# Kernel optimization log

Hardware: AMD Instinct MI355X
Metric: run time of the kernel (lower is better)

## Reference

```python
import jax, jax.numpy as jnp
import numpy as np

HIDDEN = 1024
NUM_HEADS = 16
D_HEAD = HIDDEN // NUM_HEADS  # 64
SEQ = 2048
BATCH = 2


def setup_inputs() -> dict:
    key = jax.random.key(0)
    kx, kw, kb = jax.random.split(key, 3)
    x = jax.random.normal(kx, (SEQ, BATCH, HIDDEN), dtype=jnp.float32)
    W = jax.random.normal(kw, (3 * HIDDEN, HIDDEN), dtype=jnp.float32) * 0.02
    b = jax.random.normal(kb, (3 * HIDDEN,), dtype=jnp.float32) * 0.02
    return {"x": x, "W": W, "b": b}


def reference(x, W, b):
    # x: (S, B, H) seq-first, as in the torch module
    S, B, _ = x.shape
    qkv = jnp.einsum('sbh,oh->sbo', x, W) + b  # (S, B, 3*H)
    # torch views 3*hidden as (num_heads, 3, d_head): per-head-interleaved QKV
    qkv = qkv.reshape(S, B, NUM_HEADS, 3, D_HEAD)
    qkv = jnp.transpose(qkv, (2, 1, 0, 3, 4))  # (nh, B, S, 3, d)
    q, k, v = qkv[..., 0, :], qkv[..., 1, :], qkv[..., 2, :]  # each (nh, B, S, d)
    scale = 1.0 / np.sqrt(D_HEAD).astype(np.float32)
    scores = jnp.einsum('hbqd,hbkd->hbqk', q, k) * scale  # (nh, B, S, S)
    attn = jax.nn.softmax(scores, axis=-1)
    out = jnp.einsum('hbqk,hbkd->hbqd', attn, v)  # (nh, B, S, d)
    out = jnp.transpose(out, (2, 1, 0, 3)).reshape(S, B, HIDDEN)
    return out
```

## Files before the change

kernel.cpp:

```cpp
#include <hip/hip_runtime.h>
#include <hip/hip_bf16.h>


typedef __hip_bfloat16 bf16;
typedef __bf16 bfr;
typedef __attribute__((ext_vector_type(8))) __bf16 bf16x8;
typedef __attribute__((ext_vector_type(4))) __bf16 bf16x4;
typedef __attribute__((ext_vector_type(2))) __bf16 bf16x2;
typedef __attribute__((ext_vector_type(4))) float f32x4;
typedef __attribute__((ext_vector_type(16))) float f32x16;
typedef __attribute__((ext_vector_type(4))) unsigned u32x4;

#define S_SEQ  2048
#define HID    1024
#define OUT3   3072
#define NROWS  4096

#if __has_builtin(__builtin_amdgcn_exp2f)
#define EXP2F(x) __builtin_amdgcn_exp2f(x)
#else
#define EXP2F(x) exp2f(x)
#endif

#define QSCALE 0.18033688011112042f

__global__ __launch_bounds__(256) void cast_both_kernel(
    const float* __restrict__ X, bfr* __restrict__ Xb,
    const float* __restrict__ W, bfr* __restrict__ Wb)
{
    int bid = blockIdx.x;
    const float* src;
    bfr* dst;
    int lid;
    if (bid < NROWS * HID / 2048) { src = X; dst = Xb; lid = bid; }
    else { src = W; dst = Wb; lid = bid - NROWS * HID / 2048; }
    int gid = lid * 256 + threadIdx.x;
    const float4* s4 = (const float4*)src;
    float4 a = s4[(size_t)gid * 2];
    float4 b = s4[(size_t)gid * 2 + 1];
    bf16x8 v;
    v[0] = (bfr)a.x; v[1] = (bfr)a.y; v[2] = (bfr)a.z; v[3] = (bfr)a.w;
    v[4] = (bfr)b.x; v[5] = (bfr)b.y; v[6] = (bfr)b.z; v[7] = (bfr)b.w;
    *(bf16x8*)(dst + (size_t)gid * 8) = v;
}

__device__ __forceinline__ void gload_lds16(const void* g, void* l) {
    __builtin_amdgcn_global_load_lds(
        (const __attribute__((address_space(1))) unsigned int*)g,
        (__attribute__((address_space(3))) unsigned int*)l, 16, 0, 0);
}

__global__ __launch_bounds__(256, 3) void qkv_gemm_mfma(
    const bfr* __restrict__ Xb, const bfr* __restrict__ Wb,
    const float* __restrict__ bias,
    bfr* __restrict__ qb, bfr* __restrict__ kb, bfr* __restrict__ vtb)
{
    __shared__ __attribute__((aligned(16))) unsigned char lds_all[32768];
    bfr* As = (bfr*)lds_all;
    bfr* Bs = (bfr*)(lds_all + 16384);
    bfr* Tr = (bfr*)lds_all;

    const int o0 = blockIdx.x * 128;
    const int r0 = blockIdx.y * 128;
    const int tid = threadIdx.x;
    const int lane = tid & 63;
    const int w = tid >> 6;
    const int l15 = lane & 15;
    const int quad = lane >> 4;
    const int m0 = (w & 1) * 64;
    const int n0 = (w >> 1) * 64;

    f32x4 acc[4][4];
#pragma unroll
    for (int mi = 0; mi < 4; mi++)
#pragma unroll
        for (int ni = 0; ni < 4; ni++) acc[mi][ni] = {0.f, 0.f, 0.f, 0.f};

    for (int k0 = 0; k0 < HID; k0 += 64) {
#pragma unroll
        for (int i = 0; i < 4; i++) {
            int c = i * 256 + tid;
            int row = c >> 3, c8 = c & 7;
            gload_lds16(Xb + (size_t)(r0 + row) * HID + k0 + c8 * 8, As + c * 8);
            gload_lds16(Wb + (size_t)(o0 + row) * HID + k0 + c8 * 8, Bs + c * 8);
        }
        __syncthreads();

#pragma unroll
        for (int ks = 0; ks < 2; ks++) {
            bf16x8 af[4], bfg[4];
#pragma unroll
            for (int mi = 0; mi < 4; mi++)
                af[mi] = *(const bf16x8*)(As + (m0 + mi * 16 + l15) * 64 + ks * 32 + quad * 8);
#pragma unroll
            for (int ni = 0; ni < 4; ni++)
                bfg[ni] = *(const bf16x8*)(Bs + (n0 + ni * 16 + l15) * 64 + ks * 32 + quad * 8);
#pragma unroll
            for (int mi = 0; mi < 4; mi++)
#pragma unroll
                for (int ni = 0; ni < 4; ni++)
                    acc[mi][ni] = __builtin_amdgcn_mfma_f32_16x16x32_bf16(
                        af[mi], bfg[ni], acc[mi][ni], 0, 0, 0);
        }
        __syncthreads();
    }

    const int omod = o0 % 192;
#pragma unroll
    for (int ni = 0; ni < 4; ni++) {
        int cb = o0 + n0 + ni * 16;
        int h = cb / 192;
        int rem = cb % 192;
        int t = rem >> 6;
        int d = (rem & 63) + l15;
        float bv = bias[cb + l15];
        if (t == 2) {
#pragma unroll
            for (int mi = 0; mi < 4; mi++)
#pragma unroll
                for (int r = 0; r < 4; r++) {
                    int grl = m0 + mi * 16 + quad * 4 + r;
                    Tr[(size_t)d * 144 + (grl & 1) * 72 + (grl >> 1)]
                        = (bfr)(acc[mi][ni][r] + bv);
                }
        } else {
#pragma unroll
            for (int mi = 0; mi < 4; mi++)
#pragma unroll
                for (int r = 0; r < 4; r++) {
                    int gr = r0 + m0 + mi * 16 + quad * 4 + r;
                    int s = gr >> 1, b = gr & 1;
                    int hb = h * 2 + b;
                    float val = acc[mi][ni][r] + bv;
                    if (t == 0)
                        qb[((size_t)hb * S_SEQ + s) * 64 + d] = (bfr)(val * QSCALE);
                    else
                        kb[((size_t)hb * S_SEQ + s) * 64 + d] = (bfr)val;
                }
        }
    }
    if (omod != 0) {
        __syncthreads();
        int ht = (omod == 64) ? (o0 + 64) / 192 : o0 / 192;
        int d = tid >> 2;
        int b = (tid >> 1) & 1;
        int chunk = tid & 1;
        int s0 = r0 >> 1;
        int hb = ht * 2 + b;
        const bfr* src = Tr + (size_t)d * 144 + b * 72 + chunk * 32;
        bfr* dstp = vtb + ((size_t)hb * 64 + d) * S_SEQ + s0 + chunk * 32;
#pragma unroll
        for (int j = 0; j < 4; j++)
            *(bf16x8*)(dstp + j * 8) = *(const bf16x8*)(src + j * 8);
    }
}

__device__ __forceinline__ void plswap(unsigned &a, unsigned &b) {
    asm volatile("v_permlane32_swap_b32 %0, %1" : "+v"(a), "+v"(b));
}

__global__ __launch_bounds__(256, 2) void attn32_kernel(
    const bfr* __restrict__ qb, const bfr* __restrict__ kb,
    const bfr* __restrict__ vtb, float* __restrict__ out)
{
    __shared__ __attribute__((aligned(16))) bfr KV[2][2][64 * 64];

    constexpr int NT = 32;
    const int qt = blockIdx.x;
    const int hb = blockIdx.y;
    const int h = hb >> 1, b = hb & 1;
    const int tid = threadIdx.x;
    const int lane = tid & 63;
    const int w = tid >> 6;
    const int l31 = lane & 31;
    const int hi = lane >> 5;
    const size_t hboff = (size_t)hb * S_SEQ * 64;

    const int srow = tid >> 3;
    const int slot = tid & 7;

    const int qrow = qt * 128 + w * 32 + l31;
    bf16x8 qf[4];
#pragma unroll
    for (int kk = 0; kk < 4; kk++)
        qf[kk] = *(const bf16x8*)(qb + hboff + (size_t)qrow * 64 + kk * 16 + hi * 8);

    f32x16 Oacc[2];
#pragma unroll
    for (int dt = 0; dt < 2; dt++)
#pragma unroll
        for (int i = 0; i < 16; i++) Oacc[dt][i] = 0.f;
    float lsum = 0.f;

#define STAGE(t_) do {                                                         \
    int kt__ = (t_); int bf__ = kt__ & 1;                                      \
    _Pragma("unroll")                                                          \
    for (int i = 0; i < 2; i++) {                                              \
        int r = i * 32 + srow;                                                 \
        int gc = slot ^ (r & 7);                                               \
        gload_lds16(kb + hboff + (size_t)(kt__ * 64 + r) * 64 + gc * 8,        \
                    (bfr*)&KV[bf__][0][0] + i * 2048 + tid * 8);               \
    }                                                                          \
    _Pragma("unroll")                                                          \
    for (int i = 0; i < 2; i++) {                                              \
        int r = i * 32 + srow;                                                 \
        int gc = slot ^ (r & 7);                                               \
        gload_lds16(vtb + hboff + (size_t)r * S_SEQ + kt__ * 64 + gc * 8,      \
                    (bfr*)&KV[bf__][1][0] + i * 2048 + tid * 8);               \
    }                                                                          \
} while (0)

    STAGE(0);

    for (int t = 0; t < NT; t++) {
        asm volatile("s_waitcnt vmcnt(0)" ::: "memory");
        __builtin_amdgcn_s_barrier();
        if (t + 1 < NT) STAGE(t + 1);

        const bfr* Kb = &KV[t & 1][0][0];
        const bfr* Vb = &KV[t & 1][1][0];

        unsigned wds[2][8];
        float rs = 0.f;
#pragma unroll
        for (int ts = 0; ts < 2; ts++) {
            const int krow = ts * 32 + l31;
            f32x16 sc;
#pragma unroll
            for (int i = 0; i < 16; i++) sc[i] = 0.f;
#pragma unroll
            for (int kk = 0; kk < 4; kk++) {
                int ks = (kk * 2 + hi) ^ (krow & 7);
                bf16x8 kf = *(const bf16x8*)(Kb + krow * 64 + ks * 8);
                sc = __builtin_amdgcn_mfma_f32_32x32x16_bf16(kf, qf[kk], sc, 0, 0, 0);
            }
#pragma unroll
            for (int a = 0; a < 8; a++) {
                float p0 = EXP2F(sc[2 * a]);
                float p1 = EXP2F(sc[2 * a + 1]);
                rs += p0 + p1;
                bf16x2 pk; pk[0] = (bfr)p0; pk[1] = (bfr)p1;
                wds[ts][a] = __builtin_bit_cast(unsigned, pk);
            }
        }
        lsum += rs;

        bf16x8 pfrag[4];
#pragma unroll
        for (int c = 0; c < 4; c++) {
            int ts = c >> 1, cc = c & 1;
            unsigned w0 = wds[ts][cc * 4 + 0];
            unsigned w1 = wds[ts][cc * 4 + 1];
            unsigned w2 = wds[ts][cc * 4 + 2];
            unsigned w3 = wds[ts][cc * 4 + 3];
            plswap(w0, w2);
            plswap(w1, w3);
            u32x4 pw; pw[0] = w0; pw[1] = w1; pw[2] = w2; pw[3] = w3;
            pfrag[c] = __builtin_bit_cast(bf16x8, pw);
        }

#pragma unroll
        for (int kk = 0; kk < 4; kk++)
#pragma unroll
            for (int dt = 0; dt < 2; dt++) {
                int vrow = dt * 32 + l31;
                int vs = (kk * 2 + hi) ^ (vrow & 7);
                bf16x8 vf = *(const bf16x8*)(Vb + vrow * 64 + vs * 8);
                Oacc[dt] = __builtin_amdgcn_mfma_f32_32x32x16_bf16(vf, pfrag[kk], Oacc[dt], 0, 0, 0);
            }
    }
#undef STAGE

    lsum += __shfl_xor(lsum, 32);
    float inv = 1.0f / lsum;
    float* orow = out + ((size_t)qrow * 2 + b) * HID + h * 64;
#pragma unroll
    for (int dt = 0; dt < 2; dt++)
#pragma unroll
        for (int g = 0; g < 4; g++) {
            float4 o4;
            o4.x = Oacc[dt][4 * g + 0] * inv;
            o4.y = Oacc[dt][4 * g + 1] * inv;
            o4.z = Oacc[dt][4 * g + 2] * inv;
            o4.w = Oacc[dt][4 * g + 3] * inv;
            *(float4*)(orow + dt * 32 + 8 * g + 4 * hi) = o4;
        }
}

extern "C" void kernel_launch(void* const* d_in, const int* in_sizes, int n_in,
                              void* d_out, int out_size, void* d_ws, size_t ws_size,
                              hipStream_t stream) {
    const float* X    = (const float*)d_in[0];
    const float* W    = (const float*)d_in[1];
    const float* bias = (const float*)d_in[2];
    float* out = (float*)d_out;

    bfr* qb  = (bfr*)d_ws;
    bfr* kb  = qb + (size_t)32 * S_SEQ * 64;
    bfr* vtb = kb + (size_t)32 * S_SEQ * 64;

    bfr* Xb = (bfr*)d_out;
    bfr* Wb = Xb + (size_t)NROWS * HID;

    cast_both_kernel<<<(NROWS * HID + OUT3 * HID) / 2048, 256, 0, stream>>>(X, Xb, W, Wb);

    dim3 g1(OUT3 / 128, NROWS / 128);
    qkv_gemm_mfma<<<g1, 256, 0, stream>>>(Xb, Wb, bias, qb, kb, vtb);

    dim3 g2(S_SEQ / 128, 32);
    attn32_kernel<<<g2, 256, 0, stream>>>(qb, kb, vtb, out);
}
```

Measured before the change: 157.7 us.

## Process two 32-row query tiles per wave in attention, halving block threads

Measured after the change: 175.3 us. 1.11x slower.

```diff
diff --git a/kernel.cpp b/kernel.cpp
--- a/kernel.cpp
+++ b/kernel.cpp
@@ -159,7 +159,7 @@
     asm volatile("v_permlane32_swap_b32 %0, %1" : "+v"(a), "+v"(b));
 }
 
-__global__ __launch_bounds__(256, 2) void attn32_kernel(
+__global__ __launch_bounds__(128, 2) void attn32_kernel(
     const bfr* __restrict__ qb, const bfr* __restrict__ kb,
     const bfr* __restrict__ vtb, float* __restrict__ out)
 {
@@ -179,34 +179,39 @@
     const int srow = tid >> 3;
     const int slot = tid & 7;
 
-    const int qrow = qt * 128 + w * 32 + l31;
-    bf16x8 qf[4];
-#pragma unroll
-    for (int kk = 0; kk < 4; kk++)
-        qf[kk] = *(const bf16x8*)(qb + hboff + (size_t)qrow * 64 + kk * 16 + hi * 8);
-
-    f32x16 Oacc[2];
+    const int qbase = qt * 128 + w * 64;
+    bf16x8 qf[2][4];
+#pragma unroll
+    for (int qh = 0; qh < 2; qh++)
+#pragma unroll
+        for (int kk = 0; kk < 4; kk++)
+            qf[qh][kk] = *(const bf16x8*)(qb + hboff
+                + (size_t)(qbase + qh * 32 + l31) * 64 + kk * 16 + hi * 8);
+
+    f32x16 Oacc[2][2];
 #pragma unroll
     for (int dt = 0; dt < 2; dt++)
 #pragma unroll
-        for (int i = 0; i < 16; i++) Oacc[dt][i] = 0.f;
-    float lsum = 0.f;
+        for (int qh = 0; qh < 2; qh++)
+#pragma unroll
+            for (int i = 0; i < 16; i++) Oacc[dt][qh][i] = 0.f;
+    float lsum0 = 0.f, lsum1 = 0.f;
 
 #define STAGE(t_) do {                                                         \
     int kt__ = (t_); int bf__ = kt__ & 1;                                      \
     _Pragma("unroll")                                                          \
-    for (int i = 0; i < 2; i++) {                                              \
-        int r = i * 32 + srow;                                                 \
+    for (int i = 0; i < 4; i++) {                                              \
+        int r = i * 16 + srow;                                                 \
         int gc = slot ^ (r & 7);                                               \
         gload_lds16(kb + hboff + (size_t)(kt__ * 64 + r) * 64 + gc * 8,        \
-                    (bfr*)&KV[bf__][0][0] + i * 2048 + tid * 8);               \
+                    (bfr*)&KV[bf__][0][0] + i * 1024 + tid * 8);               \
     }                                                                          \
     _Pragma("unroll")                                                          \
-    for (int i = 0; i < 2; i++) {                                              \
-        int r = i * 32 + srow;                                                 \
+    for (int i = 0; i < 4; i++) {                                              \
+        int r = i * 16 + srow;                                                 \
         int gc = slot ^ (r & 7);                                               \
         gload_lds16(vtb + hboff + (size_t)r * S_SEQ + kt__ * 64 + gc * 8,      \
-                    (bfr*)&KV[bf__][1][0] + i * 2048 + tid * 8);               \
+                    (bfr*)&KV[bf__][1][0] + i * 1024 + tid * 8);               \
     }                                                                          \
 } while (0)
 
@@ -220,43 +225,62 @@
         const bfr* Kb = &KV[t & 1][0][0];
         const bfr* Vb = &KV[t & 1][1][0];
 
-        unsigned wds[2][8];
-        float rs = 0.f;
+        unsigned wds0[2][8], wds1[2][8];
+        float rs0 = 0.f, rs1 = 0.f;
 #pragma unroll
         for (int ts = 0; ts < 2; ts++) {
             const int krow = ts * 32 + l31;
-            f32x16 sc;
-#pragma unroll
-            for (int i = 0; i < 16; i++) sc[i] = 0.f;
+            f32x16 sc0, sc1;
+#pragma unroll
+            for (int i = 0; i < 16; i++) { sc0[i] = 0.f; sc1[i] = 0.f; }
 #pragma unroll
             for (int kk = 0; kk < 4; kk++) {
                 int ks = (kk * 2 + hi) ^ (krow & 7);
                 bf16x8 kf = *(const bf16x8*)(Kb + krow * 64 + ks * 8);
-                sc = __builtin_amdgcn_mfma_f32_32x32x16_bf16(kf, qf[kk], sc, 0, 0, 0);
+                sc0 = __builtin_amdgcn_mfma_f32_32x32x16_bf16(kf, qf[0][kk], sc0, 0, 0, 0);
+                sc1 = __builtin_amdgcn_mfma_f32_32x32x16_bf16(kf, qf[1][kk], sc1, 0, 0, 0);
             }
 #pragma unroll
             for (int a = 0; a < 8; a++) {
-                float p0 = EXP2F(sc[2 * a]);
-                float p1 = EXP2F(sc[2 * a + 1]);
-                rs += p0 + p1;
-                bf16x2 pk; pk[0] = (bfr)p0; pk[1] = (bfr)p1;
-                wds[ts][a] = __builtin_bit_cast(unsigned, pk);
-            }
-        }
-        lsum += rs;
-
-        bf16x8 pfrag[4];
+                float p0 = EXP2F(sc0[2 * a]);
+                float p1 = EXP2F(sc0[2 * a + 1]);
+                rs0 += p0 + p1;
+                bf16x2 pk0; pk0[0] = (bfr)p0; pk0[1] = (bfr)p1;
+                wds0[ts][a] = __builtin_bit_cast(unsigned, pk0);
+                float p2 = EXP2F(sc1[2 * a]);
+                float p3 = EXP2F(sc1[2 * a + 1]);
+                rs1 += p2 + p3;
+                bf16x2 pk1; pk1[0] = (bfr)p2; pk1[1] = (bfr)p3;
+                wds1[ts][a] = __builtin_bit_cast(unsigned, pk1);
+            }
+        }
+        lsum0 += rs0;
+        lsum1 += rs1;
+
+        bf16x8 pfrag0[4], pfrag1[4];
 #pragma unroll
         for (int c = 0; c < 4; c++) {
             int ts = c >> 1, cc = c & 1;
-            unsigned w0 = wds[ts][cc * 4 + 0];
-            unsigned w1 = wds[ts][cc * 4 + 1];
-            unsigned w2 = wds[ts][cc * 4 + 2];
-            unsigned w3 = wds[ts][cc * 4 + 3];
-            plswap(w0, w2);
-            plswap(w1, w3);
-            u32x4 pw; pw[0] = w0; pw[1] = w1; pw[2] = w2; pw[3] = w3;
-            pfrag[c] = __builtin_bit_cast(bf16x8, pw);
+            {
+                unsigned w0 = wds0[ts][cc * 4 + 0];
+                unsigned w1 = wds0[ts][cc * 4 + 1];
+                unsigned w2 = wds0[ts][cc * 4 + 2];
+                unsigned w3 = wds0[ts][cc * 4 + 3];
+                plswap(w0, w2);
+                plswap(w1, w3);
+                u32x4 pw; pw[0] = w0; pw[1] = w1; pw[2] = w2; pw[3] = w3;
+                pfrag0[c] = __builtin_bit_cast(bf16x8, pw);
+            }
+            {
+                unsigned w0 = wds1[ts][cc * 4 + 0];
+                unsigned w1 = wds1[ts][cc * 4 + 1];
+                unsigned w2 = wds1[ts][cc * 4 + 2];
+                unsigned w3 = wds1[ts][cc * 4 + 3];
+                plswap(w0, w2);
+                plswap(w1, w3);
+                u32x4 pw; pw[0] = w0; pw[1] = w1; pw[2] = w2; pw[3] = w3;
+                pfrag1[c] = __builtin_bit_cast(bf16x8, pw);
+            }
         }
 
 #pragma unroll
@@ -266,25 +290,31 @@
                 int vrow = dt * 32 + l31;
                 int vs = (kk * 2 + hi) ^ (vrow & 7);
                 bf16x8 vf = *(const bf16x8*)(Vb + vrow * 64 + vs * 8);
-                Oacc[dt] = __builtin_amdgcn_mfma_f32_32x32x16_bf16(vf, pfrag[kk], Oacc[dt], 0, 0, 0);
+                Oacc[dt][0] = __builtin_amdgcn_mfma_f32_32x32x16_bf16(vf, pfrag0[kk], Oacc[dt][0], 0, 0, 0);
+                Oacc[dt][1] = __builtin_amdgcn_mfma_f32_32x32x16_bf16(vf, pfrag1[kk], Oacc[dt][1], 0, 0, 0);
             }
     }
 #undef STAGE
 
-    lsum += __shfl_xor(lsum, 32);
-    float inv = 1.0f / lsum;
-    float* orow = out + ((size_t)qrow * 2 + b) * HID + h * 64;
-#pragma unroll
-    for (int dt = 0; dt < 2; dt++)
-#pragma unroll
-        for (int g = 0; g < 4; g++) {
-            float4 o4;
-            o4.x = Oacc[dt][4 * g + 0] * inv;
-            o4.y = Oacc[dt][4 * g + 1] * inv;
-            o4.z = Oacc[dt][4 * g + 2] * inv;
-            o4.w = Oacc[dt][4 * g + 3] * inv;
-            *(float4*)(orow + dt * 32 + 8 * g + 4 * hi) = o4;
-        }
+    lsum0 += __shfl_xor(lsum0, 32);
+    lsum1 += __shfl_xor(lsum1, 32);
+#pragma unroll
+    for (int qh = 0; qh < 2; qh++) {
+        float inv = 1.0f / (qh == 0 ? lsum0 : lsum1);
+        int qrow = qbase + qh * 32 + l31;
+        float* orow = out + ((size_t)qrow * 2 + b) * HID + h * 64;
+#pragma unroll
+        for (int dt = 0; dt < 2; dt++)
+#pragma unroll
+            for (int g = 0; g < 4; g++) {
+                float4 o4;
+                o4.x = Oacc[dt][qh][4 * g + 0] * inv;
+                o4.y = Oacc[dt][qh][4 * g + 1] * inv;
+                o4.z = Oacc[dt][qh][4 * g + 2] * inv;
+                o4.w = Oacc[dt][qh][4 * g + 3] * inv;
+                *(float4*)(orow + dt * 32 + 8 * g + 4 * hi) = o4;
+            }
+    }
 }
 
 extern "C" void kernel_launch(void* const* d_in, const int* in_sizes, int n_in,
@@ -308,5 +338,5 @@
     qkv_gemm_mfma<<<g1, 256, 0, stream>>>(Xb, Wb, bias, qb, kb, vtb);
 
     dim3 g2(S_SEQ / 128, 32);
-    attn32_kernel<<<g2, 256, 0, stream>>>(qb, kb, vtb, out);
-}
+    attn32_kernel<<<g2, 128, 0, stream>>>(qb, kb, vtb, out);
+}
```
